# Kernel tuning notes

Measured on AMD Instinct MI355X. Metric: run time of the kernel, lower is better.

Reference implementation:

```python
import jax, jax.numpy as jnp
import numpy as np

N_NODES = 100000
N_EDGES = 1250000
IN_DIM, HID_DIM, OUT_DIM = 128, 64, 64
NUM_LAYERS = 3
EPS = 1e-12  # F.normalize eps


def setup_inputs() -> dict:
    key = jax.random.key(0)
    ks = jax.random.split(key, 10)
    s = 0.05
    x = jax.random.normal(ks[0], (N_NODES, IN_DIM), dtype=jnp.float32)
    edge_index = jax.random.randint(ks[1], (2, N_EDGES), 0, N_NODES, dtype=jnp.int32)
    W1 = jax.random.normal(ks[2], (IN_DIM, HID_DIM), dtype=jnp.float32) * s
    b1 = jax.random.normal(ks[3], (HID_DIM,), dtype=jnp.float32) * s
    Wl = jax.random.normal(ks[4], (NUM_LAYERS, HID_DIM, HID_DIM), dtype=jnp.float32) * s
    bl = jax.random.normal(ks[5], (NUM_LAYERS, HID_DIM), dtype=jnp.float32) * s
    Wr = jax.random.normal(ks[6], (NUM_LAYERS, HID_DIM, HID_DIM), dtype=jnp.float32) * s
    W2 = jax.random.normal(ks[7], (HID_DIM, OUT_DIM), dtype=jnp.float32) * s
    b2 = jax.random.normal(ks[8], (OUT_DIM,), dtype=jnp.float32) * s
    return {"x": x, "edge_index": edge_index, "W1": W1, "b1": b1,
            "Wl": Wl, "bl": bl, "Wr": Wr, "W2": W2, "b2": b2}


def reference(x, edge_index, W1, b1, Wl, bl, Wr, W2, b2):
    n = x.shape[0]
    src, dst = edge_index[0], edge_index[1]
    # in-degree for mean aggregation (zero-degree -> aggregate stays 0)
    deg = jax.ops.segment_sum(jnp.ones_like(dst, dtype=x.dtype), dst, num_segments=n)
    inv_deg = jnp.where(deg > 0, 1.0 / jnp.maximum(deg, 1.0), 0.0)[:, None]  # [n,1]
    h = x @ W1 + b1  # [n, hid]
    for i in range(Wl.shape[0]):
        # gather source features, scatter-mean to destinations
        agg = jax.ops.segment_sum(h[src], dst, num_segments=n) * inv_deg  # [n, hid]
        o = agg @ Wl[i] + bl[i] + h @ Wr[i]
        # row-wise L2 normalize (PyG normalize=True)
        norm = jnp.sqrt(jnp.sum(o * o, axis=-1, keepdims=True))
        o = o / jnp.maximum(norm, EPS)
        h = jax.nn.relu(o)
    return h @ W2 + b2
```

## Files before the change

### kernel.cpp

```cpp
#include <hip/hip_runtime.h>
#include <hip/hip_bf16.h>


#define NT 256
#define BATCH 4096
#define SBCAP 8192
#define HSTRIDE 72
#define WCONV_BLOCKS 144

typedef __attribute__((ext_vector_type(8))) short bf16x8;
typedef __attribute__((ext_vector_type(4))) float f32x4;

__device__ __forceinline__ float bfbits2f(unsigned short b) {
    return __uint_as_float(((unsigned)b) << 16);
}
__device__ __forceinline__ unsigned short f2bfbits(float v) {
    __hip_bfloat16 b = __float2bfloat16(v);
    return *reinterpret_cast<unsigned short*>(&b);
}


__global__ void zero_kernel(unsigned* __restrict__ p, int nwords) {
    const int i = blockIdx.x * blockDim.x + threadIdx.x;
    if (i < nwords) p[i] = 0u;
}


__global__ __launch_bounds__(NT) void wconv_bin1_kernel(
    const float* __restrict__ W1, const float* __restrict__ Wl,
    const float* __restrict__ Wr, const float* __restrict__ W2,
    unsigned short* __restrict__ wt,
    const int* __restrict__ src, const int* __restrict__ dst, int m,
    unsigned* __restrict__ gcur, unsigned* __restrict__ bins) {
    const int t = threadIdx.x;
    if ((int)blockIdx.x < WCONV_BLOCKS) {
        const int i = blockIdx.x * NT + t;
        if (i >= 36864) return;
        float v;
        if (i < 8192) {
            const int col = i >> 7, k = i & 127;
            v = W1[k * 64 + col];
        } else if (i < 32768) {
            const int j = i - 8192;
            const int mm = j >> 13, r = j & 8191;
            const int isR = (r >> 12) & 1, q = r & 4095;
            const int col = q >> 6, k = q & 63;
            v = (isR ? Wr : Wl)[mm * 4096 + k * 64 + col];
        } else {
            const int q = i - 32768;
            const int col = q >> 6, k = q & 63;
            v = W2[k * 64 + col];
        }
        wt[i] = f2bfbits(v);
        return;
    }
    __shared__ unsigned hist[256];
    __shared__ unsigned gbase[256];
    const int bb = (int)blockIdx.x - WCONV_BLOCKS;
    const int base = bb * BATCH;
    hist[t] = 0;
    __syncthreads();
    int d[16], s[16];
    const int e0 = base + t * 16;
    const bool full = (base + BATCH) <= m;
    if (full) {
        #pragma unroll
        for (int q = 0; q < 4; ++q) {
            const int4 dv = *(const int4*)&dst[e0 + q * 4];
            const int4 sv = *(const int4*)&src[e0 + q * 4];
            d[q*4+0]=dv.x; d[q*4+1]=dv.y; d[q*4+2]=dv.z; d[q*4+3]=dv.w;
            s[q*4+0]=sv.x; s[q*4+1]=sv.y; s[q*4+2]=sv.z; s[q*4+3]=sv.w;
        }
        #pragma unroll
        for (int q = 0; q < 16; ++q) atomicAdd(&hist[d[q] >> 9], 1u);
    } else {
        #pragma unroll
        for (int q = 0; q < 16; ++q) {
            const int e = e0 + q;
            if (e < m) { d[q] = dst[e]; s[q] = src[e]; atomicAdd(&hist[d[q] >> 9], 1u); }
            else d[q] = -1;
        }
    }
    __syncthreads();
    {
        const unsigned h = hist[t];
        gbase[t] = h ? atomicAdd(&gcur[t], h) : 0u;
        hist[t] = 0;
    }
    __syncthreads();
    if (full) {
        #pragma unroll
        for (int q = 0; q < 16; ++q) {
            const int b = d[q] >> 9;
            const unsigned slot = gbase[b] + atomicAdd(&hist[b], 1u);
            bins[(size_t)b * SBCAP + slot] = ((unsigned)s[q] << 9) | (unsigned)(d[q] & 511);
        }
    } else {
        #pragma unroll
        for (int q = 0; q < 16; ++q) {
            if (d[q] >= 0) {
                const int b = d[q] >> 9;
                const unsigned slot = gbase[b] + atomicAdd(&hist[b], 1u);
                bins[(size_t)b * SBCAP + slot] = ((unsigned)s[q] << 9) | (unsigned)(d[q] & 511);
            }
        }
    }
}


__device__ __forceinline__ void lin1_body(const float* __restrict__ x,
    const unsigned short* __restrict__ W1t, const float* __restrict__ b1,
    unsigned short* __restrict__ hbf, int n, int bid) {
    const int t = threadIdx.x;
    const int lane = t & 63;
    const int w = t >> 6;
    const int r16 = lane & 15;
    const int g = lane >> 4;
    const int row0 = bid * 128 + w * 32;

    f32x4 acc[2][4];
    #pragma unroll
    for (int i = 0; i < 2; ++i)
        #pragma unroll
        for (int j = 0; j < 4; ++j) { acc[i][j][0]=0.f; acc[i][j][1]=0.f; acc[i][j][2]=0.f; acc[i][j][3]=0.f; }

    int ra[2];
    #pragma unroll
    for (int rt = 0; rt < 2; ++rt) {
        const int r = row0 + rt * 16 + r16;
        ra[rt] = (r < n) ? r : (n - 1);
    }

    #pragma unroll 1
    for (int kc = 0; kc < 128; kc += 32) {
        bf16x8 af[2];
        #pragma unroll
        for (int rt = 0; rt < 2; ++rt) {
            const float* p = &x[(size_t)ra[rt] * 128 + kc + g * 8];
            const float4 f0 = *(const float4*)p;
            const float4 f1 = *(const float4*)(p + 4);
            bf16x8 a;
            a[0] = (short)f2bfbits(f0.x); a[1] = (short)f2bfbits(f0.y);
            a[2] = (short)f2bfbits(f0.z); a[3] = (short)f2bfbits(f0.w);
            a[4] = (short)f2bfbits(f1.x); a[5] = (short)f2bfbits(f1.y);
            a[6] = (short)f2bfbits(f1.z); a[7] = (short)f2bfbits(f1.w);
            af[rt] = a;
        }
        #pragma unroll
        for (int ct = 0; ct < 4; ++ct) {
            const bf16x8 bw = *(const bf16x8*)&W1t[(size_t)(ct * 16 + r16) * 128 + kc + g * 8];
            acc[0][ct] = __builtin_amdgcn_mfma_f32_16x16x32_bf16(af[0], bw, acc[0][ct], 0, 0, 0);
            acc[1][ct] = __builtin_amdgcn_mfma_f32_16x16x32_bf16(af[1], bw, acc[1][ct], 0, 0, 0);
        }
    }

    float bcol[4];
    #pragma unroll
    for (int ct = 0; ct < 4; ++ct) bcol[ct] = b1[ct * 16 + r16];
    #pragma unroll
    for (int rt = 0; rt < 2; ++rt) {
        const int rbase = row0 + rt * 16 + g * 4;
        #pragma unroll
        for (int reg = 0; reg < 4; ++reg) {
            const int rr = rbase + reg;
            if (rr < n) {
                #pragma unroll
                for (int ct = 0; ct < 4; ++ct)
                    hbf[(size_t)rr * 64 + ct * 16 + r16] = f2bfbits(acc[rt][ct][reg] + bcol[ct]);
            }
        }
    }
}

__global__ __launch_bounds__(NT) void bin2_lin1_kernel(
    const unsigned* __restrict__ bins, const unsigned* __restrict__ gcur,
    int* __restrict__ row_ptr, int* __restrict__ csr, int n, int nsb, int m,
    const float* __restrict__ x, const unsigned short* __restrict__ W1t,
    const float* __restrict__ b1, unsigned short* __restrict__ hbf) {
    __shared__ unsigned hist[512];
    __shared__ unsigned off[512];
    __shared__ unsigned cur[512];
    __shared__ unsigned wsum[4];
    __shared__ unsigned gpre[256];
    const int t = threadIdx.x;
    if ((int)blockIdx.x >= nsb) {
        lin1_body(x, W1t, b1, hbf, n, (int)blockIdx.x - nsb);
        return;
    }
    const int k = blockIdx.x;
    const int lane = t & 63, wid = t >> 6;

    {
        const unsigned gv = (t < nsb) ? gcur[t] : 0u;
        unsigned gx = gv;
        #pragma unroll
        for (int o = 1; o < 64; o <<= 1) {
            const unsigned tt = __shfl_up(gx, o, 64);
            if (lane >= o) gx += tt;
        }
        if (lane == 63) wsum[wid] = gx;
        __syncthreads();
        unsigned wo = 0;
        for (int w = 0; w < wid; ++w) wo += wsum[w];
        gpre[t] = wo + gx - gv;
        __syncthreads();
    }
    const int cnt = (int)gcur[k];
    const unsigned sb = gpre[k];
    if (k == 0 && t == 0) row_ptr[n] = m;

    const unsigned* reg = bins + (size_t)k * SBCAP;
    hist[2*t] = 0; hist[2*t+1] = 0;
    __syncthreads();
    for (int i = t; i < cnt; i += NT) atomicAdd(&hist[reg[i] & 511u], 1u);
    __syncthreads();
    const unsigned v0 = hist[2*t], v1 = hist[2*t+1];
    const unsigned ps = v0 + v1;
    unsigned x2 = ps;
    #pragma unroll
    for (int o = 1; o < 64; o <<= 1) {
        const unsigned tt = __shfl_up(x2, o, 64);
        if (lane >= o) x2 += tt;
    }
    if (lane == 63) wsum[wid] = x2;
    __syncthreads();
    unsigned woff = 0;
    for (int w = 0; w < wid; ++w) woff += wsum[w];
    const unsigned excl = woff + x2 - ps;
    off[2*t] = excl; off[2*t+1] = excl + v0;
    cur[2*t] = 0; cur[2*t+1] = 0;
    const int node = k * 512 + 2 * t;
    if (node < n)     row_ptr[node]     = (int)(sb + excl);
    if (node + 1 < n) row_ptr[node + 1] = (int)(sb + excl + v0);
    __syncthreads();
    for (int i = t; i < cnt; i += NT) {
        const unsigned u = reg[i];
        const unsigned l = u & 511u;
        const unsigned r = atomicAdd(&cur[l], 1u);
        csr[sb + off[l] + r] = (int)(u >> 9);
    }
}


__global__ __launch_bounds__(NT) void agg_kernel(const unsigned short* __restrict__ h,
    const int* __restrict__ row_ptr, const int* __restrict__ csr,
    unsigned short* __restrict__ aggB, int n) {
    const int t = threadIdx.x;
    const int lane = t & 63;
    const int half = lane >> 5;
    const int gs = (lane >> 4) & 1;
    const int c = lane & 15;
    const int gw = (blockIdx.x * NT + t) >> 6;
    const int nw = (gridDim.x * NT) >> 6;
    const int npairs = (n + 1) >> 1;
    for (int p = gw; p < npairs; p += nw) {
        const int node = p * 2 + half;
        const bool valid = node < n;
        const int node_c = valid ? node : (n - 1);
        const int rs = row_ptr[node_c];
        const int re = row_ptr[node_c + 1];
        float a0 = 0.f, a1 = 0.f, a2 = 0.f, a3 = 0.f;
        {
            int ce[8], si[8];
            #pragma unroll
            for (int i = 0; i < 8; ++i) {
                const int e = rs + 2 * i + gs;
                ce[i] = (e < re) ? e : 0;
            }
            #pragma unroll
            for (int i = 0; i < 8; ++i) si[i] = csr[ce[i]];
            ushort4 v[8];
            #pragma unroll
            for (int i = 0; i < 8; ++i) v[i] = *(const ushort4*)&h[(size_t)si[i] * 64 + c * 4];
            #pragma unroll
            for (int i = 0; i < 8; ++i) {
                if (rs + 2 * i + gs < re) {
                    a0 += bfbits2f(v[i].x);
                    a1 += bfbits2f(v[i].y);
                    a2 += bfbits2f(v[i].z);
                    a3 += bfbits2f(v[i].w);
                }
            }
        }
        for (int base = rs + 16; base < re; base += 8) {
            int ce[4], si[4];
            #pragma unroll
            for (int i = 0; i < 4; ++i) {
                const int e = base + 2 * i + gs;
                ce[i] = (e < re) ? e : 0;
            }
            #pragma unroll
            for (int i = 0; i < 4; ++i) si[i] = csr[ce[i]];
            ushort4 v[4];
            #pragma unroll
            for (int i = 0; i < 4; ++i) v[i] = *(const ushort4*)&h[(size_t)si[i] * 64 + c * 4];
            #pragma unroll
            for (int i = 0; i < 4; ++i) {
                if (base + 2 * i + gs < re) {
                    a0 += bfbits2f(v[i].x);
                    a1 += bfbits2f(v[i].y);
                    a2 += bfbits2f(v[i].z);
                    a3 += bfbits2f(v[i].w);
                }
            }
        }
        a0 += __shfl_xor(a0, 16, 64);
        a1 += __shfl_xor(a1, 16, 64);
        a2 += __shfl_xor(a2, 16, 64);
        a3 += __shfl_xor(a3, 16, 64);
        if (gs == 0 && valid) {
            const float inv = (re > rs) ? (1.0f / (float)(re - rs)) : 0.0f;
            ushort4 o;
            o.x = f2bfbits(a0 * inv);
            o.y = f2bfbits(a1 * inv);
            o.z = f2bfbits(a2 * inv);
            o.w = f2bfbits(a3 * inv);
            *(ushort4*)&aggB[(size_t)node * 64 + c * 4] = o;
        }
    }
}


template<int LAST>
__global__ __launch_bounds__(NT) void gemm_mfma(
    const unsigned short* __restrict__ A1b, const unsigned short* __restrict__ W1t,
    const unsigned short* __restrict__ A2b, const unsigned short* __restrict__ W2t,
    const float* __restrict__ bias, float* __restrict__ outF,
    unsigned short* __restrict__ outB, int n,
    const unsigned short* __restrict__ W2t2, const float* __restrict__ b2) {
    const int t = threadIdx.x;
    const int lane = t & 63;
    const int w = t >> 6;
    const int r16 = lane & 15;
    const int g = lane >> 4;
    const int row0 = blockIdx.x * 128 + w * 32;

    f32x4 acc[2][4];
    #pragma unroll
    for (int i = 0; i < 2; ++i)
        #pragma unroll
        for (int j = 0; j < 4; ++j) {
            acc[i][j][0] = 0.f; acc[i][j][1] = 0.f; acc[i][j][2] = 0.f; acc[i][j][3] = 0.f;
        }

    int ra[2];
    #pragma unroll
    for (int rt = 0; rt < 2; ++rt) {
        int r = row0 + rt * 16 + r16;
        ra[rt] = (r < n) ? r : (n - 1);
    }

    #pragma unroll
    for (int kc = 0; kc < 64; kc += 32) {
        bf16x8 a1[2], a2[2];
        #pragma unroll
        for (int rt = 0; rt < 2; ++rt) {
            a1[rt] = *(const bf16x8*)&A1b[(size_t)ra[rt] * 64 + kc + g * 8];
            a2[rt] = *(const bf16x8*)&A2b[(size_t)ra[rt] * 64 + kc + g * 8];
        }
        #pragma unroll
        for (int ct = 0; ct < 4; ++ct) {
            const bf16x8 bw1 = *(const bf16x8*)&W1t[(size_t)(ct * 16 + r16) * 64 + kc + g * 8];
            const bf16x8 bw2 = *(const bf16x8*)&W2t[(size_t)(ct * 16 + r16) * 64 + kc + g * 8];
            acc[0][ct] = __builtin_amdgcn_mfma_f32_16x16x32_bf16(a1[0], bw1, acc[0][ct], 0, 0, 0);
            acc[0][ct] = __builtin_amdgcn_mfma_f32_16x16x32_bf16(a2[0], bw2, acc[0][ct], 0, 0, 0);
            acc[1][ct] = __builtin_amdgcn_mfma_f32_16x16x32_bf16(a1[1], bw1, acc[1][ct], 0, 0, 0);
            acc[1][ct] = __builtin_amdgcn_mfma_f32_16x16x32_bf16(a2[1], bw2, acc[1][ct], 0, 0, 0);
        }
    }

    float bcol[4];
    #pragma unroll
    for (int ct = 0; ct < 4; ++ct) bcol[ct] = bias[ct * 16 + r16];

    #pragma unroll
    for (int rt = 0; rt < 2; ++rt) {
        #pragma unroll
        for (int ct = 0; ct < 4; ++ct)
            #pragma unroll
            for (int reg = 0; reg < 4; ++reg) acc[rt][ct][reg] += bcol[ct];

        #pragma unroll
        for (int reg = 0; reg < 4; ++reg) {
            float ss = 0.f;
            #pragma unroll
            for (int ct = 0; ct < 4; ++ct) ss += acc[rt][ct][reg] * acc[rt][ct][reg];
            ss += __shfl_xor(ss, 1, 64);
            ss += __shfl_xor(ss, 2, 64);
            ss += __shfl_xor(ss, 4, 64);
            ss += __shfl_xor(ss, 8, 64);
            const float inv = 1.0f / fmaxf(sqrtf(ss), 1e-12f);
            #pragma unroll
            for (int ct = 0; ct < 4; ++ct)
                acc[rt][ct][reg] = fmaxf(acc[rt][ct][reg] * inv, 0.0f);
        }
    }

    if constexpr (!LAST) {
        #pragma unroll
        for (int rt = 0; rt < 2; ++rt) {
            const int rbase = row0 + rt * 16 + g * 4;
            #pragma unroll
            for (int reg = 0; reg < 4; ++reg) {
                const int rr = rbase + reg;
                if (rr < n) {
                    #pragma unroll
                    for (int ct = 0; ct < 4; ++ct)
                        outB[(size_t)rr * 64 + ct * 16 + r16] = f2bfbits(acc[rt][ct][reg]);
                }
            }
        }
    } else {
        __shared__ unsigned short h3S[128][HSTRIDE];
        #pragma unroll
        for (int rt = 0; rt < 2; ++rt) {
            #pragma unroll
            for (int reg = 0; reg < 4; ++reg) {
                const int lr = w * 32 + rt * 16 + g * 4 + reg;
                #pragma unroll
                for (int ct = 0; ct < 4; ++ct)
                    h3S[lr][ct * 16 + r16] = f2bfbits(acc[rt][ct][reg]);
            }
        }
        __syncthreads();
        f32x4 acc2[2][4];
        #pragma unroll
        for (int i = 0; i < 2; ++i)
            #pragma unroll
            for (int j = 0; j < 4; ++j) { acc2[i][j][0]=0.f; acc2[i][j][1]=0.f; acc2[i][j][2]=0.f; acc2[i][j][3]=0.f; }
        #pragma unroll
        for (int kc = 0; kc < 64; kc += 32) {
            bf16x8 af[2];
            #pragma unroll
            for (int rt = 0; rt < 2; ++rt)
                af[rt] = *(const bf16x8*)&h3S[w * 32 + rt * 16 + r16][kc + g * 8];
            #pragma unroll
            for (int ct = 0; ct < 4; ++ct) {
                const bf16x8 bw = *(const bf16x8*)&W2t2[(size_t)(ct * 16 + r16) * 64 + kc + g * 8];
                acc2[0][ct] = __builtin_amdgcn_mfma_f32_16x16x32_bf16(af[0], bw, acc2[0][ct], 0, 0, 0);
                acc2[1][ct] = __builtin_amdgcn_mfma_f32_16x16x32_bf16(af[1], bw, acc2[1][ct], 0, 0, 0);
            }
        }
        float b2c[4];
        #pragma unroll
        for (int ct = 0; ct < 4; ++ct) b2c[ct] = b2[ct * 16 + r16];
        #pragma unroll
        for (int rt = 0; rt < 2; ++rt) {
            const int rbase = row0 + rt * 16 + g * 4;
            #pragma unroll
            for (int reg = 0; reg < 4; ++reg) {
                const int rr = rbase + reg;
                if (rr < n) {
                    #pragma unroll
                    for (int ct = 0; ct < 4; ++ct)
                        outF[(size_t)rr * 64 + ct * 16 + r16] = acc2[rt][ct][reg] + b2c[ct];
                }
            }
        }
    }
}


extern "C" void kernel_launch(void* const* d_in, const int* in_sizes, int n_in,
                              void* d_out, int out_size, void* d_ws, size_t ws_size,
                              hipStream_t stream) {
    const float* x  = (const float*)d_in[0];
    const int*   ei = (const int*)  d_in[1];
    const float* W1 = (const float*)d_in[2];
    const float* b1 = (const float*)d_in[3];
    const float* Wl = (const float*)d_in[4];
    const float* bl = (const float*)d_in[5];
    const float* Wr = (const float*)d_in[6];
    const float* W2 = (const float*)d_in[7];
    const float* b2 = (const float*)d_in[8];
    float* out = (float*)d_out;

    const int n = in_sizes[0] / 128;
    const int m = in_sizes[1] / 2;
    const int* src = ei;
    const int* dst = ei + m;

    const int nsb = (n + 511) >> 9;

    char* ws = (char*)d_ws;
    size_t off = 0;
    auto alloc = [&](size_t bytes) -> void* {
        void* p = ws + off;
        off = (off + bytes + 255) & ~(size_t)255;
        return p;
    };
    unsigned short* aggB    = (unsigned short*)alloc((size_t)n * 64 * 2);
    unsigned short* hbf     = (unsigned short*)alloc((size_t)n * 64 * 2);
    int*            row_ptr = (int*)alloc((size_t)(n + 1) * sizeof(int));
    unsigned*       gcur    = (unsigned*)alloc((size_t)nsb * 4);
    unsigned*       bins    = (unsigned*)alloc((size_t)nsb * SBCAP * 4);
    int*            csr     = (int*)alloc((size_t)m * 4);
    unsigned short* wt      = (unsigned short*)alloc(36864 * 2);

    const unsigned short* W1t = wt;
    const unsigned short* W2t = wt + 32768;

    const int nb1 = (m + BATCH - 1) / BATCH;
    const int gtiles = (n + 127) / 128;

    zero_kernel<<<1, NT, 0, stream>>>(gcur, nsb);

    wconv_bin1_kernel<<<WCONV_BLOCKS + nb1, NT, 0, stream>>>(W1, Wl, Wr, W2, wt,
                                                             src, dst, m, gcur, bins);
    bin2_lin1_kernel<<<nsb + gtiles, NT, 0, stream>>>(bins, gcur, row_ptr, csr, n, nsb, m,
                                                      x, W1t, b1, hbf);

    for (int i = 0; i < 2; ++i) {
        agg_kernel<<<2048, NT, 0, stream>>>(hbf, row_ptr, csr, aggB, n);
        const unsigned short* Wlt = wt + 8192 + (size_t)i * 8192;
        const unsigned short* Wrt = Wlt + 4096;
        gemm_mfma<0><<<gtiles, NT, 0, stream>>>(aggB, Wlt, hbf, Wrt,
                                                bl + (size_t)i * 64,
                                                nullptr, hbf, n, nullptr, nullptr);
    }
    agg_kernel<<<2048, NT, 0, stream>>>(hbf, row_ptr, csr, aggB, n);
    gemm_mfma<1><<<gtiles, NT, 0, stream>>>(aggB, wt + 8192 + 16384,
                                            hbf, wt + 8192 + 16384 + 4096,
                                            bl + 128, out, nullptr, n, W2t, b2);
}
```

Baseline: 189.0 us.

## Aggregate four nodes per wavefront with 16-lane groups, 16 edges per batch

The mean-aggregation kernel now maps each 16-lane group to its own node, so a wavefront handles four nodes instead of two. The old scheme split each node's edges across two half-groups and combined them with a cross-lane shuffle. Each group now walks all of its node's edges serially in batches of 16 gathered loads, which removes the shuffle reduction and the predicated output lanes. This trades shorter per-node latency for more nodes in flight per wave, and it raises register use for the 16-entry buffers. Average degree is about 12, so most nodes finish in a single batch.

Measured after the change: 202.8 us. +7.3%, slower.

```diff
diff --git a/kernel.cpp b/kernel.cpp
--- a/kernel.cpp
+++ b/kernel.cpp
@@ -247,34 +247,32 @@
     unsigned short* __restrict__ aggB, int n) {
     const int t = threadIdx.x;
     const int lane = t & 63;
-    const int half = lane >> 5;
-    const int gs = (lane >> 4) & 1;
+    const int q = lane >> 4;
     const int c = lane & 15;
     const int gw = (blockIdx.x * NT + t) >> 6;
     const int nw = (gridDim.x * NT) >> 6;
-    const int npairs = (n + 1) >> 1;
-    for (int p = gw; p < npairs; p += nw) {
-        const int node = p * 2 + half;
+    const int nquads = (n + 3) >> 2;
+    for (int p = gw; p < nquads; p += nw) {
+        const int node = p * 4 + q;
         const bool valid = node < n;
         const int node_c = valid ? node : (n - 1);
         const int rs = row_ptr[node_c];
         const int re = row_ptr[node_c + 1];
         float a0 = 0.f, a1 = 0.f, a2 = 0.f, a3 = 0.f;
-        {
-            int ce[8], si[8];
-            #pragma unroll
-            for (int i = 0; i < 8; ++i) {
-                const int e = rs + 2 * i + gs;
-                ce[i] = (e < re) ? e : 0;
-            }
-            #pragma unroll
-            for (int i = 0; i < 8; ++i) si[i] = csr[ce[i]];
-            ushort4 v[8];
-            #pragma unroll
-            for (int i = 0; i < 8; ++i) v[i] = *(const ushort4*)&h[(size_t)si[i] * 64 + c * 4];
-            #pragma unroll
-            for (int i = 0; i < 8; ++i) {
-                if (rs + 2 * i + gs < re) {
+        for (int base = rs; base < re; base += 16) {
+            int si[16];
+            #pragma unroll
+            for (int i = 0; i < 16; ++i) {
+                const int e = base + i;
+                si[i] = csr[(e < re) ? e : rs];
+            }
+            ushort4 v[16];
+            #pragma unroll
+            for (int i = 0; i < 16; ++i)
+                v[i] = *(const ushort4*)&h[(size_t)si[i] * 64 + c * 4];
+            #pragma unroll
+            for (int i = 0; i < 16; ++i) {
+                if (base + i < re) {
                     a0 += bfbits2f(v[i].x);
                     a1 += bfbits2f(v[i].y);
                     a2 += bfbits2f(v[i].z);
@@ -282,33 +280,7 @@
                 }
             }
         }
-        for (int base = rs + 16; base < re; base += 8) {
-            int ce[4], si[4];
-            #pragma unroll
-            for (int i = 0; i < 4; ++i) {
-                const int e = base + 2 * i + gs;
-                ce[i] = (e < re) ? e : 0;
-            }
-            #pragma unroll
-            for (int i = 0; i < 4; ++i) si[i] = csr[ce[i]];
-            ushort4 v[4];
-            #pragma unroll
-            for (int i = 0; i < 4; ++i) v[i] = *(const ushort4*)&h[(size_t)si[i] * 64 + c * 4];
-            #pragma unroll
-            for (int i = 0; i < 4; ++i) {
-                if (base + 2 * i + gs < re) {
-                    a0 += bfbits2f(v[i].x);
-                    a1 += bfbits2f(v[i].y);
-                    a2 += bfbits2f(v[i].z);
-                    a3 += bfbits2f(v[i].w);
-                }
-            }
-        }
-        a0 += __shfl_xor(a0, 16, 64);
-        a1 += __shfl_xor(a1, 16, 64);
-        a2 += __shfl_xor(a2, 16, 64);
-        a3 += __shfl_xor(a3, 16, 64);
-        if (gs == 0 && valid) {
+        if (valid) {
             const float inv = (re > rs) ? (1.0f / (float)(re - rs)) : 0.0f;
             ushort4 o;
             o.x = f2bfbits(a0 * inv);
```
